# Performance work log

Hardware: AMD Instinct MI355X
Metric: run time of the kernel (lower is better)

## Reference

```python
import jax, jax.numpy as jnp
import numpy as np

EMBED_DIM = 1024
NUM_HEADS = 16
NUM_GROUPS = 4
HEAD_DIM = EMBED_DIM // NUM_HEADS
REPEAT = NUM_HEADS // NUM_GROUPS
MAX_TIME = 128
MAX_FREQ = 8


def build_relative_index(q_len, k_len, freq_size=MAX_FREQ, max_time=MAX_TIME, max_freq=MAX_FREQ):
    # static (numpy) construction; shapes are compile-time constants under jit
    q_time = q_len // max_freq
    k_time = k_len // max_freq
    qt = np.arange(q_time) + (k_time - q_time)
    q_coords = np.stack(np.meshgrid(qt, np.arange(freq_size), indexing='ij')).reshape(2, -1)
    k_coords = np.stack(np.meshgrid(np.arange(k_time), np.arange(freq_size), indexing='ij')).reshape(2, -1)
    rel = q_coords[:, :, None] - k_coords[:, None, :]  # [2, Nq, Nk]
    rel_t = np.clip(rel[0], -max_time + 1, max_time - 1) + max_time - 1
    rel_f = np.clip(rel[1], -max_freq + 1, max_freq - 1) + max_freq - 1
    return jnp.asarray(rel_t, jnp.int32), jnp.asarray(rel_f, jnp.int32)


def setup_inputs() -> dict:
    key = jax.random.key(0)
    ks = jax.random.split(key, 11)
    B, N, D, Nc = 2, 512, EMBED_DIM, 1536
    s = 0.02
    return {
        'q': jax.random.normal(ks[0], (B, N, D), jnp.float32),
        'k': jax.random.normal(ks[1], (B, N, D), jnp.float32),
        'v': jax.random.normal(ks[2], (B, N, D), jnp.float32),
        'attn_cache_k': jax.random.normal(ks[3], (B * NUM_HEADS, HEAD_DIM, Nc), jnp.float32),
        'attn_cache_v': jax.random.normal(ks[4], (B * NUM_HEADS, Nc, HEAD_DIM), jnp.float32),
        'Wq': jax.random.normal(ks[5], (D, D), jnp.float32) * s,
        'Wk': jax.random.normal(ks[6], (D, HEAD_DIM * NUM_GROUPS), jnp.float32) * s,
        'Wv': jax.random.normal(ks[7], (D, HEAD_DIM * NUM_GROUPS), jnp.float32) * s,
        'Wo': jax.random.normal(ks[8], (D, D), jnp.float32) * s,
        'emb_t': jax.random.normal(ks[9], (2 * MAX_TIME - 1, HEAD_DIM), jnp.float32) * s,
        'emb_f': jax.random.normal(ks[10], (2 * MAX_FREQ - 1, HEAD_DIM), jnp.float32) * s,
    }


def reference(q, k, v, attn_cache_k, attn_cache_v, Wq, Wk, Wv, Wo, emb_t, emb_f):
    B, N, D = q.shape
    H, G, hd, r = NUM_HEADS, NUM_GROUPS, HEAD_DIM, REPEAT
    # projections (no bias); head layout matches torch view: [B, N, H, hd] -> [B*H, N, hd]
    qp = (q @ Wq).reshape(B, N, H, hd).transpose(0, 2, 1, 3).reshape(B * H, N, hd)
    kp = (k @ Wk).reshape(B, N, G, hd).transpose(0, 2, 3, 1).reshape(B * G, hd, N)  # transposed K
    vp = (v @ Wv).reshape(B, N, G, hd).transpose(0, 2, 1, 3).reshape(B * G, N, hd)
    # GQA: repeat_interleave kv heads to query heads
    kp = jnp.repeat(kp, r, axis=0)
    vp = jnp.repeat(vp, r, axis=0)
    # streaming cache concat + slide
    k_full = jnp.concatenate([attn_cache_k, kp], axis=-1)            # [B*H, hd, Nk]
    new_cache_k = k_full[:, :, -attn_cache_k.shape[-1]:]
    v_full = jnp.concatenate([attn_cache_v, vp], axis=1)             # [B*H, Nk, hd]
    new_cache_v = v_full[:, -attn_cache_v.shape[1]:, :]
    Nk = k_full.shape[-1]
    qs = qp * (hd ** -0.5)
    scores = jnp.einsum('bid,bdj->bij', qs, k_full)                  # [B*H, N, Nk]
    rel_t, rel_f = build_relative_index(N, Nk)
    rel_emb = emb_t[rel_t] + emb_f[rel_f]                            # [N, Nk, hd]
    bias = jnp.einsum('bid,ijd->bij', qs, rel_emb)
    attn = jax.nn.softmax(scores + bias, axis=-1)
    ao = jnp.einsum('bij,bjd->bid', attn, v_full)                    # [B*H, N, hd]
    ao = ao.reshape(B, H, N, hd).transpose(2, 0, 1, 3).reshape(N, B, D)
    out = (ao @ Wo).transpose(1, 0, 2)                               # [B, N, D]
    return out, new_cache_k, new_cache_v
```

## Files before the change

### kernel.cpp

```cpp
#include <hip/hip_runtime.h>
#include <math.h>

typedef _Float16 half_t;
typedef _Float16 half8  __attribute__((ext_vector_type(8)));
typedef _Float16 half4v __attribute__((ext_vector_type(4)));
typedef float    floatx4 __attribute__((ext_vector_type(4)));

#define LOG2E 1.44269504088896f

static __device__ __forceinline__ floatx4 mfma16(half8 a, half8 b, floatx4 c) {
    return __builtin_amdgcn_mfma_f32_16x16x32_f16(a, b, c, 0, 0, 0);
}
static __device__ __forceinline__ floatx4 mfma16x16(half4v a, half4v b, floatx4 c) {
    return __builtin_amdgcn_mfma_f32_16x16x16f16(a, b, c, 0, 0, 0);
}

__global__ __launch_bounds__(256) void prepw(const float* __restrict__ Wq,
                                             const float* __restrict__ Wk,
                                             const float* __restrict__ Wv,
                                             const float* __restrict__ Wo,
                                             const float* __restrict__ emb_t,
                                             const float* __restrict__ emb_f,
                                             half_t* __restrict__ WqT,
                                             half_t* __restrict__ WkvT,
                                             half_t* __restrict__ WoT,
                                             half_t* __restrict__ embc)
{
    const int tid = threadIdx.x;
    const int id = blockIdx.x;
    __shared__ float t[64][65];
    const float* src; half_t* dst; int Ncols, n0, k0;
    if (id < 256)      { src = Wq; dst = WqT; Ncols = 1024; n0 = (id & 15) * 64; k0 = (id >> 4) * 64; }
    else if (id < 320) { int q2 = id - 256; src = Wk; dst = WkvT; Ncols = 256; n0 = (q2 & 3) * 64; k0 = (q2 >> 2) * 64; }
    else if (id < 384) { int q2 = id - 320; src = Wv; dst = WkvT + 256 * 1024; Ncols = 256; n0 = (q2 & 3) * 64; k0 = (q2 >> 2) * 64; }
    else if (id < 640) { int q2 = id - 384; src = Wo; dst = WoT; Ncols = 1024; n0 = (q2 & 15) * 64; k0 = (q2 >> 4) * 64; }
    else {
        int idx = (id - 640) * 256 + tid;
        int row = idx >> 6, col = idx & 63;
        float val = 0.f;
        if (row < 255) val = emb_t[row * 64 + col];
        else if (row >= 256 && row < 271) val = emb_f[(row - 256) * 64 + col];
        embc[idx] = (half_t)val;
        return;
    }
    #pragma unroll
    for (int i2 = 0; i2 < 4; i2++) {
        int idx = i2 * 256 + tid;
        int r = idx >> 4, c4 = (idx & 15) * 4;
        *(float4*)&t[r][c4] = *(const float4*)&src[(size_t)(k0 + r) * Ncols + n0 + c4];
    }
    __syncthreads();
    #pragma unroll
    for (int i2 = 0; i2 < 2; i2++) {
        int idx = i2 * 256 + tid;
        int n = idx >> 3, kb = (idx & 7) * 8;
        half8 o;
        #pragma unroll
        for (int u = 0; u < 8; u++) o[u] = (half_t)t[kb + u][n];
        *(half8*)&dst[(size_t)(n0 + n) * 1024 + k0 + kb] = o;
    }
}

static __device__ __forceinline__ void proj_core(int task, int m0, int n0,
                                                 const float* __restrict__ Af,
                                                 const half_t* __restrict__ Ah,
                                                 const half_t* __restrict__ Bt,
                                                 half_t* __restrict__ qs_h,
                                                 half_t* __restrict__ kp_h,
                                                 half_t* __restrict__ Vp4,
                                                 float* __restrict__ out,
                                                 float* __restrict__ out_k,
                                                 float* __restrict__ out_v,
                                                 half_t* sm, int tid)
{
    half_t* As = sm;
    half_t* Bs = sm + 4 * 4608;

    const int kh = tid >> 8, t8 = tid & 255;
    const int w4 = (tid >> 6) & 3, l = tid & 63;
    const int quad = l >> 4, lr = l & 15, wm = w4 >> 1, wn = w4 & 1;
    const int arow = t8 >> 2, acol = (t8 & 3) * 16;
    const int kbase = kh * 512;
    half_t* Ak = As + kh * 2 * 4608;
    half_t* Bk = Bs + kh * 2 * 4608;

    {
        int kk = kbase;
        if (Af) {
            float4 f0 = *(const float4*)&Af[(size_t)(m0 + arow) * 1024 + kk + acol];
            float4 f1 = *(const float4*)&Af[(size_t)(m0 + arow) * 1024 + kk + acol + 4];
            float4 f2 = *(const float4*)&Af[(size_t)(m0 + arow) * 1024 + kk + acol + 8];
            float4 f3 = *(const float4*)&Af[(size_t)(m0 + arow) * 1024 + kk + acol + 12];
            half8 h0, h1;
            h0[0]=(half_t)f0.x; h0[1]=(half_t)f0.y; h0[2]=(half_t)f0.z; h0[3]=(half_t)f0.w;
            h0[4]=(half_t)f1.x; h0[5]=(half_t)f1.y; h0[6]=(half_t)f1.z; h0[7]=(half_t)f1.w;
            h1[0]=(half_t)f2.x; h1[1]=(half_t)f2.y; h1[2]=(half_t)f2.z; h1[3]=(half_t)f2.w;
            h1[4]=(half_t)f3.x; h1[5]=(half_t)f3.y; h1[6]=(half_t)f3.z; h1[7]=(half_t)f3.w;
            *(half8*)&Ak[arow * 72 + acol] = h0;
            *(half8*)&Ak[arow * 72 + acol + 8] = h1;
        } else {
            *(half8*)&Ak[arow * 72 + acol]     = *(const half8*)&Ah[(size_t)(m0 + arow) * 1024 + kk + acol];
            *(half8*)&Ak[arow * 72 + acol + 8] = *(const half8*)&Ah[(size_t)(m0 + arow) * 1024 + kk + acol + 8];
        }
        *(half8*)&Bk[arow * 72 + acol]     = *(const half8*)&Bt[(size_t)(n0 + arow) * 1024 + kk + acol];
        *(half8*)&Bk[arow * 72 + acol + 8] = *(const half8*)&Bt[(size_t)(n0 + arow) * 1024 + kk + acol + 8];
    }
    __syncthreads();

    floatx4 zero = {0.f, 0.f, 0.f, 0.f};
    floatx4 acc[2][2];
    acc[0][0] = zero; acc[0][1] = zero; acc[1][0] = zero; acc[1][1] = zero;

    float4 pf0, pf1, pf2, pf3; half8 ph0, ph1, pb0, pb1;
    for (int it = 0; it < 8; ++it) {
        if (it < 7) {
            int kk = kbase + (it + 1) * 64;
            if (Af) {
                pf0 = *(const float4*)&Af[(size_t)(m0 + arow) * 1024 + kk + acol];
                pf1 = *(const float4*)&Af[(size_t)(m0 + arow) * 1024 + kk + acol + 4];
                pf2 = *(const float4*)&Af[(size_t)(m0 + arow) * 1024 + kk + acol + 8];
                pf3 = *(const float4*)&Af[(size_t)(m0 + arow) * 1024 + kk + acol + 12];
            } else {
                ph0 = *(const half8*)&Ah[(size_t)(m0 + arow) * 1024 + kk + acol];
                ph1 = *(const half8*)&Ah[(size_t)(m0 + arow) * 1024 + kk + acol + 8];
            }
            pb0 = *(const half8*)&Bt[(size_t)(n0 + arow) * 1024 + kk + acol];
            pb1 = *(const half8*)&Bt[(size_t)(n0 + arow) * 1024 + kk + acol + 8];
        }
        const half_t* Ab = Ak + (it & 1) * 4608;
        const half_t* Bb = Bk + (it & 1) * 4608;
        #pragma unroll
        for (int ks = 0; ks < 2; ++ks) {
            half8 a0 = *(const half8*)&Ab[(wm * 32 + lr) * 72 + ks * 32 + quad * 8];
            half8 a1 = *(const half8*)&Ab[(wm * 32 + 16 + lr) * 72 + ks * 32 + quad * 8];
            half8 b0 = *(const half8*)&Bb[(wn * 32 + lr) * 72 + ks * 32 + quad * 8];
            half8 b1 = *(const half8*)&Bb[(wn * 32 + 16 + lr) * 72 + ks * 32 + quad * 8];
            acc[0][0] = mfma16(a0, b0, acc[0][0]);
            acc[0][1] = mfma16(a0, b1, acc[0][1]);
            acc[1][0] = mfma16(a1, b0, acc[1][0]);
            acc[1][1] = mfma16(a1, b1, acc[1][1]);
        }
        __syncthreads();
        if (it < 7) {
            int buf = (it + 1) & 1;
            if (Af) {
                half8 h0, h1;
                h0[0]=(half_t)pf0.x; h0[1]=(half_t)pf0.y; h0[2]=(half_t)pf0.z; h0[3]=(half_t)pf0.w;
                h0[4]=(half_t)pf1.x; h0[5]=(half_t)pf1.y; h0[6]=(half_t)pf1.z; h0[7]=(half_t)pf1.w;
                h1[0]=(half_t)pf2.x; h1[1]=(half_t)pf2.y; h1[2]=(half_t)pf2.z; h1[3]=(half_t)pf2.w;
                h1[4]=(half_t)pf3.x; h1[5]=(half_t)pf3.y; h1[6]=(half_t)pf3.z; h1[7]=(half_t)pf3.w;
                *(half8*)&Ak[buf * 4608 + arow * 72 + acol] = h0;
                *(half8*)&Ak[buf * 4608 + arow * 72 + acol + 8] = h1;
            } else {
                *(half8*)&Ak[buf * 4608 + arow * 72 + acol] = ph0;
                *(half8*)&Ak[buf * 4608 + arow * 72 + acol + 8] = ph1;
            }
            *(half8*)&Bk[buf * 4608 + arow * 72 + acol] = pb0;
            *(half8*)&Bk[buf * 4608 + arow * 72 + acol + 8] = pb1;
            __syncthreads();
        }
    }

    float* M = (float*)Bs;
    if (kh == 1) {
        #pragma unroll
        for (int mi = 0; mi < 2; mi++)
            #pragma unroll
            for (int ni = 0; ni < 2; ni++)
                #pragma unroll
                for (int r = 0; r < 4; r++)
                    M[(wm * 32 + mi * 16 + quad * 4 + r) * 66 + wn * 32 + ni * 16 + lr] = acc[mi][ni][r];
    }
    __syncthreads();
    if (kh == 0) {
        #pragma unroll
        for (int mi = 0; mi < 2; mi++)
            #pragma unroll
            for (int ni = 0; ni < 2; ni++)
                #pragma unroll
                for (int r = 0; r < 4; r++)
                    acc[mi][ni][r] += M[(wm * 32 + mi * 16 + quad * 4 + r) * 66 + wn * 32 + ni * 16 + lr];
    }

    if (task == 0) {
        if (kh == 0) {
            #pragma unroll
            for (int mi = 0; mi < 2; mi++)
                #pragma unroll
                for (int ni = 0; ni < 2; ni++)
                    #pragma unroll
                    for (int r = 0; r < 4; r++) {
                        int m = m0 + wm * 32 + mi * 16 + quad * 4 + r;
                        int n = n0 + wn * 32 + ni * 16 + lr;
                        qs_h[(size_t)m * 1024 + n] = (half_t)(acc[mi][ni][r] * (0.125f * LOG2E));
                    }
        }
    } else if (task == 2) {
        if (kh == 0) {
            #pragma unroll
            for (int mi = 0; mi < 2; mi++)
                #pragma unroll
                for (int ni = 0; ni < 2; ni++)
                    #pragma unroll
                    for (int r = 0; r < 4; r++) {
                        int m = m0 + wm * 32 + mi * 16 + quad * 4 + r;
                        int n = n0 + wn * 32 + ni * 16 + lr;
                        out[(size_t)m * 1024 + n] = acc[mi][ni][r];
                    }
        }
    } else {
        float* Ct = (float*)As;
        if (kh == 0) {
            #pragma unroll
            for (int mi = 0; mi < 2; mi++)
                #pragma unroll
                for (int ni = 0; ni < 2; ni++)
                    #pragma unroll
                    for (int r = 0; r < 4; r++)
                        Ct[(wn * 32 + ni * 16 + lr) * 68 + wm * 32 + mi * 16 + quad * 4 + r] = acc[mi][ni][r];
        }
        __syncthreads();
        if (kh == 0) {
            const int b = m0 >> 9, jm0 = m0 & 511;
            if (n0 < 256) {
                int gg = n0 >> 6;
                {
                    int d = t8 >> 2, jc = (t8 & 3) * 16;
                    float4 vv[4];
                    #pragma unroll
                    for (int u = 0; u < 4; u++) vv[u] = *(float4*)&Ct[d * 68 + jc + u * 4];
                    #pragma unroll
                    for (int t = 0; t < 4; t++)
                        #pragma unroll
                        for (int u = 0; u < 4; u++)
                            *(float4*)&out_k[((size_t)((b * 16 + gg * 4 + t) * 64 + d)) * 1536 + 1024 + jm0 + jc + u * 4] = vv[u];
                }
                {
                    int j = t8 >> 2, dc = (t8 & 3) * 16;
                    half8 o0, o1;
                    #pragma unroll
                    for (int u = 0; u < 8; u++) o0[u] = (half_t)Ct[(dc + u) * 68 + j];
                    #pragma unroll
                    for (int u = 0; u < 8; u++) o1[u] = (half_t)Ct[(dc + 8 + u) * 68 + j];
                    *(half8*)&kp_h[((size_t)(b * 512 + jm0 + j)) * 256 + n0 + dc] = o0;
                    *(half8*)&kp_h[((size_t)(b * 512 + jm0 + j)) * 256 + n0 + dc + 8] = o1;
                }
            } else {
                int gg = (n0 - 256) >> 6;
                {
                    int j = t8 >> 2, dc = (t8 & 3) * 16;
                    float4 vv[4];
                    #pragma unroll
                    for (int u = 0; u < 4; u++) {
                        float4 x;
                        x.x = Ct[(dc + u * 4 + 0) * 68 + j];
                        x.y = Ct[(dc + u * 4 + 1) * 68 + j];
                        x.z = Ct[(dc + u * 4 + 2) * 68 + j];
                        x.w = Ct[(dc + u * 4 + 3) * 68 + j];
                        vv[u] = x;
                    }
                    #pragma unroll
                    for (int t = 0; t < 4; t++)
                        #pragma unroll
                        for (int u = 0; u < 4; u++)
                            *(float4*)&out_v[(((size_t)(b * 16 + gg * 4 + t) * 1536) + 1024 + jm0 + j) * 64 + dc + u * 4] = vv[u];
                }
                {
                    int d = t8 >> 2, jc16 = (t8 & 3) * 16;
                    #pragma unroll
                    for (int u = 0; u < 4; u++) {
                        half4v o;
                        #pragma unroll
                        for (int s2 = 0; s2 < 4; s2++) o[s2] = (half_t)Ct[d * 68 + jc16 + u * 4 + s2];
                        *(half4v*)&Vp4[(((size_t)(b * 4 + gg) * 128 + ((jm0 + jc16) >> 2) + u) * 64 + d) * 4] = o;
                    }
                }
            }
        }
    }
}

__global__ __launch_bounds__(512) void stage1(const float* __restrict__ qin,
                                              const float* __restrict__ kin,
                                              const float* __restrict__ vin,
                                              const float* __restrict__ cache_k,
                                              const float* __restrict__ cache_v,
                                              const half_t* __restrict__ WqT,
                                              const half_t* __restrict__ WkvT,
                                              half_t* __restrict__ qs_h,
                                              half_t* __restrict__ kp_h,
                                              half_t* __restrict__ Vp4,
                                              half_t* __restrict__ Kc,
                                              half_t* __restrict__ Vc4,
                                              float* __restrict__ out_k,
                                              float* __restrict__ out_v)
{
    __shared__ __align__(16) unsigned char sm[73728];
    const int bid = blockIdx.x;
    const int tid = threadIdx.x;

    if (bid < 384) {
        int task, m0, n0;
        const float* Af; const half_t* Bt;
        if (bid < 256) { task = 0; m0 = (bid >> 4) * 64; n0 = (bid & 15) * 64; Af = qin; Bt = WqT; }
        else { task = 1; int t = bid - 256; m0 = (t >> 3) * 64; n0 = (t & 7) * 64;
               Af = (n0 < 256) ? kin : vin; Bt = WkvT; }
        proj_core(task, m0, n0, Af, nullptr, Bt, qs_h, kp_h, Vp4,
                  nullptr, out_k, out_v, (half_t*)sm, tid);
        return;
    }

    const int nb = bid - 384;
    const int sub = tid >> 8, tl = tid & 255;
    const int bx = nb % 24, by = nb / 24;
    const int bh = by, j0 = bx * 64;
    const bool shift = (j0 >= 512);
    float (*t)[65] = (float(*)[65])(sm + sub * 16640);

    if (sub == 0) {
        #pragma unroll
        for (int i2 = 0; i2 < 4; i2++) {
            int idx = i2 * 256 + tl;
            int d = idx >> 4, j4 = (idx & 15) * 4;
            float4 vv = *(const float4*)&cache_k[((size_t)bh * 64 + d) * 1536 + j0 + j4];
            *(float4*)&t[d][j4] = vv;
            if (shift) *(float4*)&out_k[((size_t)bh * 64 + d) * 1536 + j0 - 512 + j4] = vv;
        }
    } else {
        #pragma unroll
        for (int i2 = 0; i2 < 4; i2++) {
            int idx = i2 * 256 + tl;
            int j = idx >> 4, d4 = (idx & 15) * 4;
            float4 vv = *(const float4*)&cache_v[((size_t)bh * 1536 + j0 + j) * 64 + d4];
            *(float4*)&t[j][d4] = vv;
            if (shift) *(float4*)&out_v[((size_t)bh * 1536 + j0 + j - 512) * 64 + d4] = vv;
        }
    }
    __syncthreads();
    if (sub == 0) {
        #pragma unroll
        for (int i2 = 0; i2 < 2; i2++) {
            int idx = i2 * 256 + tl;
            int j = idx >> 3, db = (idx & 7) * 8;
            half8 o;
            #pragma unroll
            for (int u = 0; u < 8; u++) o[u] = (half_t)t[db + u][j];
            *(half8*)&Kc[((size_t)bh * 1536 + j0 + j) * 64 + db] = o;
        }
    } else {
        #pragma unroll
        for (int i2 = 0; i2 < 4; i2++) {
            int idx = i2 * 256 + tl;
            int jc = idx >> 6, d = idx & 63;
            half4v o;
            #pragma unroll
            for (int u = 0; u < 4; u++) o[u] = (half_t)t[jc * 4 + u][d];
            *(half4v*)&Vc4[(((size_t)bh * 384 + (j0 >> 2) + jc) * 64 + d) * 4] = o;
        }
    }
}

__global__ __launch_bounds__(512) void proj1(const half_t* __restrict__ AO,
                                             const half_t* __restrict__ WoT,
                                             float* __restrict__ out)
{
    __shared__ __align__(16) unsigned char sm[73728];
    const int id = blockIdx.x;
    const int m0 = (id >> 4) * 64, n0 = (id & 15) * 64;
    proj_core(2, m0, n0, nullptr, AO, WoT, nullptr, nullptr, nullptr,
              out, nullptr, nullptr, (half_t*)sm, threadIdx.x);
}

__global__ __launch_bounds__(512, 4) void flash(const half_t* __restrict__ qs_h,
                                                const half_t* __restrict__ Kc,
                                                const half_t* __restrict__ kp_h,
                                                const half_t* __restrict__ Vc4,
                                                const half_t* __restrict__ Vp4,
                                                const half_t* __restrict__ embc,
                                                half_t* __restrict__ AO)
{
    __shared__ __align__(16) unsigned char smem_raw[61824];
    half_t* bt = (half_t*)smem_raw;

    const int bh = blockIdx.x, b = bh >> 4, h = bh & 15, g = h >> 2;
    const int i0 = blockIdx.y * 32;
    const int tid = threadIdx.x, jh = tid >> 6, l = tid & 63;
    const int quad = l >> 4, lr = l & 15;

    half8 qf[2][2];
    #pragma unroll
    for (int ih = 0; ih < 2; ih++) {
        const half_t* qsrc = &qs_h[((size_t)(b * 512 + i0 + ih * 16 + lr)) * 1024 + h * 64];
        qf[ih][0] = *(const half8*)(qsrc + quad * 8);
        qf[ih][1] = *(const half8*)(qsrc + 32 + quad * 8);
    }

    floatx4 zero = {0.f, 0.f, 0.f, 0.f};
    {
        int ih = jh & 1;
        for (int tk = 4 + (jh >> 1); tk < 17; tk += 4) {
            floatx4 acc = zero;
            half8 e0 = *(const half8*)&embc[(size_t)(tk * 16 + lr) * 64 + quad * 8];
            half8 e1 = *(const half8*)&embc[(size_t)(tk * 16 + lr) * 64 + 32 + quad * 8];
            acc = mfma16(e0, qf[ih][0], acc);
            acc = mfma16(e1, qf[ih][1], acc);
            #pragma unroll
            for (int r = 0; r < 4; r++)
                bt[(ih * 16 + lr) * 210 + tk * 16 + quad * 4 + r - 64] = (half_t)acc[r];
        }
    }
    __syncthreads();

    float bfv[2][4];
    #pragma unroll
    for (int ih = 0; ih < 2; ih++)
        #pragma unroll
        for (int r = 0; r < 4; r++) {
            int f = (lr & 7) - ((quad & 1) * 4 + r) + 7;
            bfv[ih][r] = (float)bt[(ih * 16 + lr) * 210 + 192 + f];
        }
    const int qtr0 = (i0 + lr) >> 3;
    const int qtr1 = (i0 + 16 + lr) >> 3;

    floatx4 accO[2][4];
    #pragma unroll
    for (int ih = 0; ih < 2; ih++)
        #pragma unroll
        for (int ni = 0; ni < 4; ni++) accO[ih][ni] = zero;
    floatx4 accS[2];
    accS[0] = zero; accS[1] = zero;
    const half4v vone = {(half_t)1.f, (half_t)1.f, (half_t)1.f, (half_t)1.f};

    half8 kc0, kc1; half4v vb[4];
    {
        const half_t* kb = &Kc[((size_t)bh * 1536 + jh * 16 + lr) * 64];
        kc0 = *(const half8*)(kb + quad * 8);
        kc1 = *(const half8*)(kb + 32 + quad * 8);
        const half_t* vbase = Vc4 + (size_t)bh * 98304;
        const int jc = jh * 4 + quad;
        #pragma unroll
        for (int ni = 0; ni < 4; ni++)
            vb[ni] = *(const half4v*)&vbase[((size_t)jc * 64 + ni * 16 + lr) * 4];
    }

    for (int jt = 0; jt < 16; ++jt) {
        half8 kn0, kn1; half4v vn[4];
        if (jt < 15) {
            const int j1 = (jt + 1) * 128;
            const half_t* kb = (j1 < 1536)
                ? &Kc[((size_t)bh * 1536 + j1 + jh * 16 + lr) * 64]
                : &kp_h[((size_t)(b * 512 + j1 - 1536 + jh * 16 + lr)) * 256 + g * 64];
            kn0 = *(const half8*)(kb + quad * 8);
            kn1 = *(const half8*)(kb + 32 + quad * 8);
            const half_t* vbase; int jcb;
            if (j1 < 1536) { vbase = Vc4 + (size_t)bh * 98304;          jcb = j1 >> 2; }
            else           { vbase = Vp4 + (size_t)(b * 4 + g) * 32768; jcb = (j1 - 1536) >> 2; }
            const int jc = jcb + jh * 4 + quad;
            #pragma unroll
            for (int ni = 0; ni < 4; ni++)
                vn[ni] = *(const half4v*)&vbase[((size_t)jc * 64 + ni * 16 + lr) * 4];
        }

        floatx4 s[2];
        #pragma unroll
        for (int ih = 0; ih < 2; ih++) {
            s[ih] = mfma16(kc0, qf[ih][0], zero);
            s[ih] = mfma16(kc1, qf[ih][1], s[ih]);
        }
        const int ktb = jt * 16 + jh * 2 + (quad >> 1);
        #pragma unroll
        for (int ih = 0; ih < 2; ih++) {
            int toff = 255 + (ih ? qtr1 : qtr0) - ktb;
            toff = min(toff, 190);
            float tb = (float)bt[(ih * 16 + lr) * 210 + toff];
            #pragma unroll
            for (int r = 0; r < 4; r++)
                s[ih][r] = exp2f(s[ih][r] + tb + bfv[ih][r]);
        }
        #pragma unroll
        for (int ih = 0; ih < 2; ih++) {
            half4v pf;
            #pragma unroll
            for (int r = 0; r < 4; r++) pf[r] = (half_t)s[ih][r];
            accS[ih] = mfma16x16(pf, vone, accS[ih]);
            #pragma unroll
            for (int ni = 0; ni < 4; ni++)
                accO[ih][ni] = mfma16x16(pf, vb[ni], accO[ih][ni]);
        }
        if (jt < 15) {
            kc0 = kn0; kc1 = kn1;
            #pragma unroll
            for (int ni = 0; ni < 4; ni++) vb[ni] = vn[ni];
        }
    }

    __syncthreads();
    float* Mf = (float*)smem_raw;
    float* Sf = Mf + 7 * 32 * 68;
    if (jh != 0) {
        const int p = jh - 1;
        #pragma unroll
        for (int ih = 0; ih < 2; ih++) {
            #pragma unroll
            for (int ni = 0; ni < 4; ni++)
                #pragma unroll
                for (int r = 0; r < 4; r++)
                    Mf[(p * 32 + ih * 16 + quad * 4 + r) * 68 + ni * 16 + lr] = accO[ih][ni][r];
            if (lr == 0) {
                #pragma unroll
                for (int r = 0; r < 4; r++)
                    Sf[p * 32 + ih * 16 + quad * 4 + r] = accS[ih][r];
            }
        }
    }
    __syncthreads();
    if (jh == 0) {
        #pragma unroll
        for (int ih = 0; ih < 2; ih++) {
            float inv[4];
            #pragma unroll
            for (int r = 0; r < 4; r++) {
                float t = accS[ih][r];
                #pragma unroll
                for (int p = 0; p < 7; p++) t += Sf[p * 32 + ih * 16 + quad * 4 + r];
                inv[r] = 1.0f / t;
            }
            #pragma unroll
            for (int ni = 0; ni < 4; ni++)
                #pragma unroll
                for (int r = 0; r < 4; r++) {
                    float o = accO[ih][ni][r];
                    #pragma unroll
                    for (int p = 0; p < 7; p++)
                        o += Mf[(p * 32 + ih * 16 + quad * 4 + r) * 68 + ni * 16 + lr];
                    int row = ih * 16 + quad * 4 + r;
                    AO[((size_t)(b * 512 + i0 + row)) * 1024 + h * 64 + ni * 16 + lr] =
                        (half_t)(o * inv[r]);
                }
        }
    }
}

extern "C" void kernel_launch(void* const* d_in, const int* in_sizes, int n_in,
                              void* d_out, int out_size, void* d_ws, size_t ws_size,
                              hipStream_t stream)
{
    const float* q       = (const float*)d_in[0];
    const float* k       = (const float*)d_in[1];
    const float* v       = (const float*)d_in[2];
    const float* cache_k = (const float*)d_in[3];
    const float* cache_v = (const float*)d_in[4];
    const float* Wq      = (const float*)d_in[5];
    const float* Wk      = (const float*)d_in[6];
    const float* Wv      = (const float*)d_in[7];
    const float* Wo      = (const float*)d_in[8];
    const float* emb_t   = (const float*)d_in[9];
    const float* emb_f   = (const float*)d_in[10];

    float* out   = (float*)d_out;
    float* out_k = out + 1048576;
    float* out_v = out_k + 3145728;

    half_t* ws = (half_t*)d_ws;
    half_t* qs_h = ws;
    half_t* kp_h = ws + 1048576;
    half_t* Vp4  = ws + 1310720;
    half_t* Kc   = ws + 1572864;
    half_t* Vc4  = ws + 4718592;
    half_t* WqT  = ws + 7864320;
    half_t* WkvT = ws + 8912896;
    half_t* WoT  = ws + 9437184;
    half_t* embc = ws + 10485760;
    half_t* AO   = ws + 10506240;

    prepw<<<dim3(720), 256, 0, stream>>>(Wq, Wk, Wv, Wo, emb_t, emb_f,
                                         WqT, WkvT, WoT, embc);
    stage1<<<dim3(1152), 512, 0, stream>>>(q, k, v, cache_k, cache_v,
                                           WqT, WkvT, qs_h, kp_h, Vp4,
                                           Kc, Vc4, out_k, out_v);
    flash<<<dim3(32, 16), 512, 0, stream>>>(qs_h, Kc, kp_h, Vc4, Vp4, embc, AO);
    proj1<<<dim3(256), 512, 0, stream>>>(AO, WoT, out);
}
```

Before: 169.1 us.

## Fuse all stages into one persistent cooperative kernel with grid syncs

Merges weight prep, cache conversion, QKV projection, flash attention and output projection into a single cooperative kernel of 256 persistent blocks separated by grid-wide syncs. Work items are redistributed so cache transposes run alongside weight conversion before the projections. This aims to remove kernel launch gaps and tail effects between four launches, at the cost of fewer resident blocks and lower occupancy in the attention phase plus grid-sync overhead. A fallback to four separate launches is used if the cooperative launch fails.

```diff
diff --git a/kernel.cpp b/kernel.cpp
--- a/kernel.cpp
+++ b/kernel.cpp
@@ -1,5 +1,8 @@
 #include <hip/hip_runtime.h>
+#include <hip/hip_cooperative_groups.h>
 #include <math.h>
+
+namespace cg = cooperative_groups;
 
 typedef _Float16 half_t;
 typedef _Float16 half8  __attribute__((ext_vector_type(8)));
@@ -13,52 +16,6 @@
 }
 static __device__ __forceinline__ floatx4 mfma16x16(half4v a, half4v b, floatx4 c) {
     return __builtin_amdgcn_mfma_f32_16x16x16f16(a, b, c, 0, 0, 0);
-}
-
-__global__ __launch_bounds__(256) void prepw(const float* __restrict__ Wq,
-                                             const float* __restrict__ Wk,
-                                             const float* __restrict__ Wv,
-                                             const float* __restrict__ Wo,
-                                             const float* __restrict__ emb_t,
-                                             const float* __restrict__ emb_f,
-                                             half_t* __restrict__ WqT,
-                                             half_t* __restrict__ WkvT,
-                                             half_t* __restrict__ WoT,
-                                             half_t* __restrict__ embc)
-{
-    const int tid = threadIdx.x;
-    const int id = blockIdx.x;
-    __shared__ float t[64][65];
-    const float* src; half_t* dst; int Ncols, n0, k0;
-    if (id < 256)      { src = Wq; dst = WqT; Ncols = 1024; n0 = (id & 15) * 64; k0 = (id >> 4) * 64; }
-    else if (id < 320) { int q2 = id - 256; src = Wk; dst = WkvT; Ncols = 256; n0 = (q2 & 3) * 64; k0 = (q2 >> 2) * 64; }
-    else if (id < 384) { int q2 = id - 320; src = Wv; dst = WkvT + 256 * 1024; Ncols = 256; n0 = (q2 & 3) * 64; k0 = (q2 >> 2) * 64; }
-    else if (id < 640) { int q2 = id - 384; src = Wo; dst = WoT; Ncols = 1024; n0 = (q2 & 15) * 64; k0 = (q2 >> 4) * 64; }
-    else {
-        int idx = (id - 640) * 256 + tid;
-        int row = idx >> 6, col = idx & 63;
-        float val = 0.f;
-        if (row < 255) val = emb_t[row * 64 + col];
-        else if (row >= 256 && row < 271) val = emb_f[(row - 256) * 64 + col];
-        embc[idx] = (half_t)val;
-        return;
-    }
-    #pragma unroll
-    for (int i2 = 0; i2 < 4; i2++) {
-        int idx = i2 * 256 + tid;
-        int r = idx >> 4, c4 = (idx & 15) * 4;
-        *(float4*)&t[r][c4] = *(const float4*)&src[(size_t)(k0 + r) * Ncols + n0 + c4];
-    }
-    __syncthreads();
-    #pragma unroll
-    for (int i2 = 0; i2 < 2; i2++) {
-        int idx = i2 * 256 + tid;
-        int n = idx >> 3, kb = (idx & 7) * 8;
-        half8 o;
-        #pragma unroll
-        for (int u = 0; u < 8; u++) o[u] = (half_t)t[kb + u][n];
-        *(half8*)&dst[(size_t)(n0 + n) * 1024 + k0 + kb] = o;
-    }
 }
 
 static __device__ __forceinline__ void proj_core(int task, int m0, int n0,
@@ -280,111 +237,119 @@
     }
 }
 
-__global__ __launch_bounds__(512) void stage1(const float* __restrict__ qin,
-                                              const float* __restrict__ kin,
-                                              const float* __restrict__ vin,
-                                              const float* __restrict__ cache_k,
-                                              const float* __restrict__ cache_v,
-                                              const half_t* __restrict__ WqT,
-                                              const half_t* __restrict__ WkvT,
-                                              half_t* __restrict__ qs_h,
-                                              half_t* __restrict__ kp_h,
-                                              half_t* __restrict__ Vp4,
-                                              half_t* __restrict__ Kc,
-                                              half_t* __restrict__ Vc4,
-                                              float* __restrict__ out_k,
-                                              float* __restrict__ out_v)
-{
-    __shared__ __align__(16) unsigned char sm[73728];
-    const int bid = blockIdx.x;
-    const int tid = threadIdx.x;
-
-    if (bid < 384) {
-        int task, m0, n0;
-        const float* Af; const half_t* Bt;
-        if (bid < 256) { task = 0; m0 = (bid >> 4) * 64; n0 = (bid & 15) * 64; Af = qin; Bt = WqT; }
-        else { task = 1; int t = bid - 256; m0 = (t >> 3) * 64; n0 = (t & 7) * 64;
-               Af = (n0 < 256) ? kin : vin; Bt = WkvT; }
-        proj_core(task, m0, n0, Af, nullptr, Bt, qs_h, kp_h, Vp4,
-                  nullptr, out_k, out_v, (half_t*)sm, tid);
-        return;
-    }
-
-    const int nb = bid - 384;
+static __device__ __forceinline__ void phaseA_body(int bid, int tid,
+    const float* __restrict__ cache_k, const float* __restrict__ cache_v,
+    const float* __restrict__ Wq, const float* __restrict__ Wk,
+    const float* __restrict__ Wv, const float* __restrict__ Wo,
+    const float* __restrict__ emb_t, const float* __restrict__ emb_f,
+    half_t* __restrict__ Kc, half_t* __restrict__ Vc4,
+    float* __restrict__ out_k, float* __restrict__ out_v,
+    half_t* __restrict__ WqT, half_t* __restrict__ WkvT,
+    half_t* __restrict__ WoT, half_t* __restrict__ embc,
+    unsigned char* sm)
+{
     const int sub = tid >> 8, tl = tid & 255;
-    const int bx = nb % 24, by = nb / 24;
-    const int bh = by, j0 = bx * 64;
-    const bool shift = (j0 >= 512);
     float (*t)[65] = (float(*)[65])(sm + sub * 16640);
-
-    if (sub == 0) {
-        #pragma unroll
-        for (int i2 = 0; i2 < 4; i2++) {
-            int idx = i2 * 256 + tl;
-            int d = idx >> 4, j4 = (idx & 15) * 4;
-            float4 vv = *(const float4*)&cache_k[((size_t)bh * 64 + d) * 1536 + j0 + j4];
-            *(float4*)&t[d][j4] = vv;
-            if (shift) *(float4*)&out_k[((size_t)bh * 64 + d) * 1536 + j0 - 512 + j4] = vv;
-        }
-    } else {
-        #pragma unroll
-        for (int i2 = 0; i2 < 4; i2++) {
-            int idx = i2 * 256 + tl;
-            int j = idx >> 4, d4 = (idx & 15) * 4;
-            float4 vv = *(const float4*)&cache_v[((size_t)bh * 1536 + j0 + j) * 64 + d4];
-            *(float4*)&t[j][d4] = vv;
-            if (shift) *(float4*)&out_v[((size_t)bh * 1536 + j0 + j - 512) * 64 + d4] = vv;
-        }
-    }
-    __syncthreads();
-    if (sub == 0) {
-        #pragma unroll
-        for (int i2 = 0; i2 < 2; i2++) {
-            int idx = i2 * 256 + tl;
-            int j = idx >> 3, db = (idx & 7) * 8;
-            half8 o;
-            #pragma unroll
-            for (int u = 0; u < 8; u++) o[u] = (half_t)t[db + u][j];
-            *(half8*)&Kc[((size_t)bh * 1536 + j0 + j) * 64 + db] = o;
-        }
-    } else {
-        #pragma unroll
-        for (int i2 = 0; i2 < 4; i2++) {
-            int idx = i2 * 256 + tl;
-            int jc = idx >> 6, d = idx & 63;
-            half4v o;
-            #pragma unroll
-            for (int u = 0; u < 4; u++) o[u] = (half_t)t[jc * 4 + u][d];
-            *(half4v*)&Vc4[(((size_t)bh * 384 + (j0 >> 2) + jc) * 64 + d) * 4] = o;
-        }
-    }
-}
-
-__global__ __launch_bounds__(512) void proj1(const half_t* __restrict__ AO,
-                                             const half_t* __restrict__ WoT,
-                                             float* __restrict__ out)
-{
-    __shared__ __align__(16) unsigned char sm[73728];
-    const int id = blockIdx.x;
-    const int m0 = (id >> 4) * 64, n0 = (id & 15) * 64;
-    proj_core(2, m0, n0, nullptr, AO, WoT, nullptr, nullptr, nullptr,
-              out, nullptr, nullptr, (half_t*)sm, threadIdx.x);
-}
-
-__global__ __launch_bounds__(512, 4) void flash(const half_t* __restrict__ qs_h,
-                                                const half_t* __restrict__ Kc,
-                                                const half_t* __restrict__ kp_h,
-                                                const half_t* __restrict__ Vc4,
-                                                const half_t* __restrict__ Vp4,
-                                                const half_t* __restrict__ embc,
-                                                half_t* __restrict__ AO)
-{
-    __shared__ __align__(16) unsigned char smem_raw[61824];
+    #pragma unroll 1
+    for (int r = 0; r < 5; ++r) {
+        const int u = r * 512 + bid * 2 + sub;
+        int cat = -1, p0 = 0, p1 = 0;
+        if (u < 768)       { cat = 0; p0 = u % 24; p1 = u / 24; }
+        else if (u < 1536) { cat = 1; int u2 = u - 768; p0 = u2 % 24; p1 = u2 / 24; }
+        else if (u < 2176) { cat = 2; p0 = u - 1536; }
+        else if (u < 2256) { cat = 3; p0 = u - 2176; }
+        const float* wsrc = nullptr; half_t* wdst = nullptr; int Ncols = 0, n0 = 0, k0 = 0;
+        if (cat == 2) {
+            int w = p0;
+            if (w < 256)      { wsrc = Wq; wdst = WqT; Ncols = 1024; n0 = (w & 15) * 64; k0 = (w >> 4) * 64; }
+            else if (w < 320) { int q2 = w - 256; wsrc = Wk; wdst = WkvT; Ncols = 256; n0 = (q2 & 3) * 64; k0 = (q2 >> 2) * 64; }
+            else if (w < 384) { int q2 = w - 320; wsrc = Wv; wdst = WkvT + 256 * 1024; Ncols = 256; n0 = (q2 & 3) * 64; k0 = (q2 >> 2) * 64; }
+            else              { int q2 = w - 384; wsrc = Wo; wdst = WoT; Ncols = 1024; n0 = (q2 & 15) * 64; k0 = (q2 >> 4) * 64; }
+        }
+        if (cat == 0) {
+            const int bh = p1, j0 = p0 * 64;
+            const bool shift = (j0 >= 512);
+            #pragma unroll
+            for (int i2 = 0; i2 < 4; i2++) {
+                int idx = i2 * 256 + tl;
+                int d = idx >> 4, j4 = (idx & 15) * 4;
+                float4 vv = *(const float4*)&cache_k[((size_t)bh * 64 + d) * 1536 + j0 + j4];
+                *(float4*)&t[d][j4] = vv;
+                if (shift) *(float4*)&out_k[((size_t)bh * 64 + d) * 1536 + j0 - 512 + j4] = vv;
+            }
+        } else if (cat == 1) {
+            const int bh = p1, j0 = p0 * 64;
+            const bool shift = (j0 >= 512);
+            #pragma unroll
+            for (int i2 = 0; i2 < 4; i2++) {
+                int idx = i2 * 256 + tl;
+                int j = idx >> 4, d4 = (idx & 15) * 4;
+                float4 vv = *(const float4*)&cache_v[((size_t)bh * 1536 + j0 + j) * 64 + d4];
+                *(float4*)&t[j][d4] = vv;
+                if (shift) *(float4*)&out_v[((size_t)bh * 1536 + j0 + j - 512) * 64 + d4] = vv;
+            }
+        } else if (cat == 2) {
+            #pragma unroll
+            for (int i2 = 0; i2 < 4; i2++) {
+                int idx = i2 * 256 + tl;
+                int rr = idx >> 4, c4 = (idx & 15) * 4;
+                *(float4*)&t[rr][c4] = *(const float4*)&wsrc[(size_t)(k0 + rr) * Ncols + n0 + c4];
+            }
+        } else if (cat == 3) {
+            int idx = p0 * 256 + tl;
+            int row = idx >> 6, col = idx & 63;
+            float val = 0.f;
+            if (row < 255) val = emb_t[row * 64 + col];
+            else if (row >= 256 && row < 271) val = emb_f[(row - 256) * 64 + col];
+            embc[idx] = (half_t)val;
+        }
+        __syncthreads();
+        if (cat == 0) {
+            const int bh = p1, j0 = p0 * 64;
+            #pragma unroll
+            for (int i2 = 0; i2 < 2; i2++) {
+                int idx = i2 * 256 + tl;
+                int j = idx >> 3, db = (idx & 7) * 8;
+                half8 o;
+                #pragma unroll
+                for (int uu = 0; uu < 8; uu++) o[uu] = (half_t)t[db + uu][j];
+                *(half8*)&Kc[((size_t)bh * 1536 + j0 + j) * 64 + db] = o;
+            }
+        } else if (cat == 1) {
+            const int bh = p1, j0 = p0 * 64;
+            #pragma unroll
+            for (int i2 = 0; i2 < 4; i2++) {
+                int idx = i2 * 256 + tl;
+                int jc = idx >> 6, d = idx & 63;
+                half4v o;
+                #pragma unroll
+                for (int uu = 0; uu < 4; uu++) o[uu] = (half_t)t[jc * 4 + uu][d];
+                *(half4v*)&Vc4[(((size_t)bh * 384 + (j0 >> 2) + jc) * 64 + d) * 4] = o;
+            }
+        } else if (cat == 2) {
+            #pragma unroll
+            for (int i2 = 0; i2 < 2; i2++) {
+                int idx = i2 * 256 + tl;
+                int n = idx >> 3, kb = (idx & 7) * 8;
+                half8 o;
+                #pragma unroll
+                for (int uu = 0; uu < 8; uu++) o[uu] = (half_t)t[kb + uu][n];
+                *(half8*)&wdst[(size_t)(n0 + n) * 1024 + k0 + kb] = o;
+            }
+        }
+        __syncthreads();
+    }
+}
+
+static __device__ __forceinline__ void flash_core(int bh, int i0,
+    const half_t* __restrict__ qs_h, const half_t* __restrict__ Kc,
+    const half_t* __restrict__ kp_h, const half_t* __restrict__ Vc4,
+    const half_t* __restrict__ Vp4, const half_t* __restrict__ embc,
+    half_t* __restrict__ AO, unsigned char* smem_raw, int tid)
+{
     half_t* bt = (half_t*)smem_raw;
-
-    const int bh = blockIdx.x, b = bh >> 4, h = bh & 15, g = h >> 2;
-    const int i0 = blockIdx.y * 32;
-    const int tid = threadIdx.x, jh = tid >> 6, l = tid & 63;
+    const int b = bh >> 4, h = bh & 15, g = h >> 2;
+    const int jh = tid >> 6, l = tid & 63;
     const int quad = l >> 4, lr = l & 15;
 
     half8 qf[2][2];
@@ -520,10 +485,10 @@
             float inv[4];
             #pragma unroll
             for (int r = 0; r < 4; r++) {
-                float t = accS[ih][r];
-                #pragma unroll
-                for (int p = 0; p < 7; p++) t += Sf[p * 32 + ih * 16 + quad * 4 + r];
-                inv[r] = 1.0f / t;
+                float tt = accS[ih][r];
+                #pragma unroll
+                for (int p = 0; p < 7; p++) tt += Sf[p * 32 + ih * 16 + quad * 4 + r];
+                inv[r] = 1.0f / tt;
             }
             #pragma unroll
             for (int ni = 0; ni < 4; ni++)
@@ -541,13 +506,111 @@
     }
 }
 
+static __device__ __forceinline__ void phaseB_body(int bid, int tid,
+    const float* qin, const float* kin, const float* vin,
+    const half_t* WqT, const half_t* WkvT,
+    half_t* qs_h, half_t* kp_h, half_t* Vp4,
+    float* out_k, float* out_v, unsigned char* sm)
+{
+    #pragma unroll 1
+    for (int t2 = bid; t2 < 384; t2 += 256) {
+        int task, m0, n0;
+        const float* Af; const half_t* Bt;
+        if (t2 < 256) { task = 0; m0 = (t2 >> 4) * 64; n0 = (t2 & 15) * 64; Af = qin; Bt = WqT; }
+        else { task = 1; int t3 = t2 - 256; m0 = (t3 >> 3) * 64; n0 = (t3 & 7) * 64;
+               Af = (n0 < 256) ? kin : vin; Bt = WkvT; }
+        __syncthreads();
+        proj_core(task, m0, n0, Af, nullptr, Bt, qs_h, kp_h, Vp4,
+                  nullptr, out_k, out_v, (half_t*)sm, tid);
+    }
+}
+
+static __device__ __forceinline__ void phaseC_body(int bid, int tid,
+    const half_t* qs_h, const half_t* Kc, const half_t* kp_h,
+    const half_t* Vc4, const half_t* Vp4, const half_t* embc,
+    half_t* AO, unsigned char* sm)
+{
+    #pragma unroll 1
+    for (int u = bid; u < 512; u += 256) {
+        __syncthreads();
+        flash_core(u & 31, (u >> 5) * 32, qs_h, Kc, kp_h, Vc4, Vp4, embc, AO, sm, tid);
+    }
+}
+
+__global__ __launch_bounds__(512, 2) void fused(
+    const float* __restrict__ qin, const float* __restrict__ kin,
+    const float* __restrict__ vin, const float* __restrict__ cache_k,
+    const float* __restrict__ cache_v, const float* __restrict__ Wq,
+    const float* __restrict__ Wk, const float* __restrict__ Wv,
+    const float* __restrict__ Wo, const float* __restrict__ emb_t,
+    const float* __restrict__ emb_f,
+    float* __restrict__ out, float* __restrict__ out_k, float* __restrict__ out_v,
+    half_t* __restrict__ qs_h, half_t* __restrict__ kp_h, half_t* __restrict__ Vp4,
+    half_t* __restrict__ Kc, half_t* __restrict__ Vc4,
+    half_t* __restrict__ WqT, half_t* __restrict__ WkvT, half_t* __restrict__ WoT,
+    half_t* __restrict__ embc, half_t* __restrict__ AO)
+{
+    __shared__ __align__(16) unsigned char sm[73728];
+    cg::grid_group grid = cg::this_grid();
+    const int bid = blockIdx.x, tid = threadIdx.x;
+
+    phaseA_body(bid, tid, cache_k, cache_v, Wq, Wk, Wv, Wo, emb_t, emb_f,
+                Kc, Vc4, out_k, out_v, WqT, WkvT, WoT, embc, sm);
+    grid.sync();
+    phaseB_body(bid, tid, qin, kin, vin, WqT, WkvT, qs_h, kp_h, Vp4,
+                out_k, out_v, sm);
+    grid.sync();
+    phaseC_body(bid, tid, qs_h, Kc, kp_h, Vc4, Vp4, embc, AO, sm);
+    grid.sync();
+    if (bid < 256)
+        proj_core(2, (bid >> 4) * 64, (bid & 15) * 64, nullptr, AO, WoT,
+                  nullptr, nullptr, nullptr, out, nullptr, nullptr,
+                  (half_t*)sm, tid);
+}
+
+__global__ __launch_bounds__(512, 2) void k_phaseA(
+    const float* cache_k, const float* cache_v, const float* Wq,
+    const float* Wk, const float* Wv, const float* Wo,
+    const float* emb_t, const float* emb_f,
+    half_t* Kc, half_t* Vc4, float* out_k, float* out_v,
+    half_t* WqT, half_t* WkvT, half_t* WoT, half_t* embc)
+{
+    __shared__ __align__(16) unsigned char sm[73728];
+    phaseA_body(blockIdx.x, threadIdx.x, cache_k, cache_v, Wq, Wk, Wv, Wo,
+                emb_t, emb_f, Kc, Vc4, out_k, out_v, WqT, WkvT, WoT, embc, sm);
+}
+__global__ __launch_bounds__(512, 2) void k_phaseB(
+    const float* qin, const float* kin, const float* vin,
+    const half_t* WqT, const half_t* WkvT,
+    half_t* qs_h, half_t* kp_h, half_t* Vp4, float* out_k, float* out_v)
+{
+    __shared__ __align__(16) unsigned char sm[73728];
+    phaseB_body(blockIdx.x, threadIdx.x, qin, kin, vin, WqT, WkvT,
+                qs_h, kp_h, Vp4, out_k, out_v, sm);
+}
+__global__ __launch_bounds__(512, 2) void k_phaseC(
+    const half_t* qs_h, const half_t* Kc, const half_t* kp_h,
+    const half_t* Vc4, const half_t* Vp4, const half_t* embc, half_t* AO)
+{
+    __shared__ __align__(16) unsigned char sm[73728];
+    phaseC_body(blockIdx.x, threadIdx.x, qs_h, Kc, kp_h, Vc4, Vp4, embc, AO, sm);
+}
+__global__ __launch_bounds__(512, 2) void k_phaseD(
+    const half_t* AO, const half_t* WoT, float* out)
+{
+    __shared__ __align__(16) unsigned char sm[73728];
+    proj_core(2, (blockIdx.x >> 4) * 64, (blockIdx.x & 15) * 64, nullptr, AO,
+              WoT, nullptr, nullptr, nullptr, out, nullptr, nullptr,
+              (half_t*)sm, threadIdx.x);
+}
+
 extern "C" void kernel_launch(void* const* d_in, const int* in_sizes, int n_in,
                               void* d_out, int out_size, void* d_ws, size_t ws_size,
                               hipStream_t stream)
 {
-    const float* q       = (const float*)d_in[0];
-    const float* k       = (const float*)d_in[1];
-    const float* v       = (const float*)d_in[2];
+    const float* qin     = (const float*)d_in[0];
+    const float* kin     = (const float*)d_in[1];
+    const float* vin     = (const float*)d_in[2];
     const float* cache_k = (const float*)d_in[3];
     const float* cache_v = (const float*)d_in[4];
     const float* Wq      = (const float*)d_in[5];
@@ -573,11 +636,23 @@
     half_t* embc = ws + 10485760;
     half_t* AO   = ws + 10506240;
 
-    prepw<<<dim3(720), 256, 0, stream>>>(Wq, Wk, Wv, Wo, emb_t, emb_f,
-                                         WqT, WkvT, WoT, embc);
-    stage1<<<dim3(1152), 512, 0, stream>>>(q, k, v, cache_k, cache_v,
-                                           WqT, WkvT, qs_h, kp_h, Vp4,
-                                           Kc, Vc4, out_k, out_v);
-    flash<<<dim3(32, 16), 512, 0, stream>>>(qs_h, Kc, kp_h, Vc4, Vp4, embc, AO);
-    proj1<<<dim3(256), 512, 0, stream>>>(AO, WoT, out);
-}
+    void* args[] = {
+        (void*)&qin, (void*)&kin, (void*)&vin, (void*)&cache_k, (void*)&cache_v,
+        (void*)&Wq, (void*)&Wk, (void*)&Wv, (void*)&Wo, (void*)&emb_t, (void*)&emb_f,
+        (void*)&out, (void*)&out_k, (void*)&out_v,
+        (void*)&qs_h, (void*)&kp_h, (void*)&Vp4, (void*)&Kc, (void*)&Vc4,
+        (void*)&WqT, (void*)&WkvT, (void*)&WoT, (void*)&embc, (void*)&AO
+    };
+    hipError_t e = hipLaunchCooperativeKernel((const void*)fused, dim3(256),
+                                              dim3(512), args, 0, stream);
+    if (e != hipSuccess) {
+        (void)hipGetLastError();
+        k_phaseA<<<dim3(256), 512, 0, stream>>>(cache_k, cache_v, Wq, Wk, Wv, Wo,
+                                                emb_t, emb_f, Kc, Vc4, out_k, out_v,
+                                                WqT, WkvT, WoT, embc);
+        k_phaseB<<<dim3(256), 512, 0, stream>>>(qin, kin, vin, WqT, WkvT,
+                                                qs_h, kp_h, Vp4, out_k, out_v);
+        k_phaseC<<<dim3(256), 512, 0, stream>>>(qs_h, Kc, kp_h, Vc4, Vp4, embc, AO);
+        k_phaseD<<<dim3(256), 512, 0, stream>>>(AO, WoT, out);
+    }
+}
```

Result: slower. 368.7 us (+118.1%).
